# Optimization experiments

Measured on AMD Instinct MI355X. Metric: run time of the kernel, lower is better.

Reference implementation:

```python
import jax, jax.numpy as jnp
import numpy as np

N = 50000      # num_nodes
E = 800000     # num_edges (avg degree 16)
IN, HID, OUT = 128, 64, 64


def setup_inputs() -> dict:
    key = jax.random.key(0)
    ks = jax.random.split(key, 4)
    x = jax.random.normal(ks[0], (N, IN), dtype=jnp.float32)
    edge_index = jax.random.randint(ks[1], (2, E), 0, N, dtype=jnp.int32)
    # GCNConv params: weight [in, out] and bias [out] per layer
    W1 = jax.random.normal(ks[2], (IN, HID), dtype=jnp.float32) * 0.05
    b1 = jnp.zeros((HID,), dtype=jnp.float32)
    W2 = jax.random.normal(ks[3], (HID, OUT), dtype=jnp.float32) * 0.05
    b2 = jnp.zeros((OUT,), dtype=jnp.float32)
    return {"x": x, "edge_index": edge_index, "W1": W1, "b1": b1, "W2": W2, "b2": b2}


def _gcn_conv(x, W, b, src, dst, norm, n):
    # linear transform, then normalized gather->scatter-add aggregation
    h = x @ W                                    # [N, out]
    msg = h[src] * norm[:, None]                 # [E+N, out] gathered messages
    out = jax.ops.segment_sum(msg, dst, num_segments=n)
    return out + b


def reference(x, edge_index, W1, b1, W2, b2):
    n = x.shape[0]
    # add self-loops (PyG GCNConv default)
    loop = jnp.arange(n, dtype=edge_index.dtype)
    src = jnp.concatenate([edge_index[0], loop])
    dst = jnp.concatenate([edge_index[1], loop])
    # symmetric normalization D^-1/2 A D^-1/2 (degree over destination)
    deg = jax.ops.segment_sum(jnp.ones_like(dst, dtype=x.dtype), dst, num_segments=n)
    dinv = jnp.where(deg > 0, jax.lax.rsqrt(deg), jnp.zeros_like(deg))
    norm = dinv[src] * dinv[dst]                 # [E+N]
    h = _gcn_conv(x, W1, b1, src, dst, norm, n)
    h = jax.nn.leaky_relu(h, negative_slope=0.01)
    # dropout is identity in eval mode (training=False)
    return _gcn_conv(h, W2, b2, src, dst, norm, n)
```

## Files before the change

kernel.cpp:

```cpp
#include <hip/hip_runtime.h>
#include <hip/hip_fp16.h>
#include <type_traits>


#define NBC   128
#define BSH   7
#define NBMAX 512
#define CAP   8192

typedef __bf16 bf16x8 __attribute__((ext_vector_type(8)));
typedef float  f32x4  __attribute__((ext_vector_type(4)));

__device__ __forceinline__ unsigned short f2bf(float f) {
    unsigned u = __float_as_uint(f);
    unsigned r = u + 0x7fff + ((u >> 16) & 1);
    return (unsigned short)(r >> 16);
}
__device__ __forceinline__ float bf2f(unsigned short h) {
    return __uint_as_float(((unsigned)h) << 16);
}

__global__ __launch_bounds__(256) void k_hist1(const int* __restrict__ dst,
                                               int* __restrict__ T, int E, int nbuck) {
    __shared__ int hist[NBMAX];
    for (int i = threadIdx.x; i < nbuck; i += 256) hist[i] = 0;
    __syncthreads();
    const int per = (E + NBC - 1) / NBC;
    const int beg = blockIdx.x * per, end = min(beg + per, E);
    for (int i = beg + threadIdx.x; i < end; i += 256)
        atomicAdd(&hist[dst[i] >> BSH], 1);
    __syncthreads();
    for (int b = threadIdx.x; b < nbuck; b += 256)
        T[b * NBC + blockIdx.x] = hist[b];
}

__global__ __launch_bounds__(1024) void k_bsum(const int* __restrict__ in,
                                               int* __restrict__ bsum, int m) {
    __shared__ int red[16];
    const int t = threadIdx.x;
    const int i = blockIdx.x * 1024 + t;
    int v = (i < m) ? in[i] : 0;
#pragma unroll
    for (int o = 32; o; o >>= 1) v += __shfl_down(v, o);
    if ((t & 63) == 0) red[t >> 6] = v;
    __syncthreads();
    if (t == 0) {
        int s = 0;
#pragma unroll
        for (int w = 0; w < 16; ++w) s += red[w];
        bsum[blockIdx.x] = s;
    }
}

__global__ void k_sbsum(const int* __restrict__ bsum, int* __restrict__ boff, int nb) {
    if (threadIdx.x == 0 && blockIdx.x == 0) {
        int run = 0;
        for (int i = 0; i < nb; ++i) { boff[i] = run; run += bsum[i]; }
    }
}

__global__ __launch_bounds__(1024) void k_scanexc(
    const int* __restrict__ in, const int* __restrict__ boff,
    int* __restrict__ out, int m) {
    __shared__ int sh[1024];
    const int t = threadIdx.x;
    const int i = blockIdx.x * 1024 + t;
    const int v = (i < m) ? in[i] : 0;
    sh[t] = v;
    __syncthreads();
#pragma unroll
    for (int o = 1; o < 1024; o <<= 1) {
        int add = (t >= o) ? sh[t - o] : 0;
        __syncthreads();
        sh[t] += add;
        __syncthreads();
    }
    if (i < m) out[i] = boff[blockIdx.x] + sh[t] - v;
}

__global__ __launch_bounds__(256) void k_part1(
    const int* __restrict__ src, const int* __restrict__ dst,
    const int* __restrict__ Toff, unsigned* __restrict__ stage, int E, int nbuck) {
    __shared__ int base[NBMAX];
    __shared__ int cnt[NBMAX];
    for (int i = threadIdx.x; i < nbuck; i += 256) {
        base[i] = Toff[i * NBC + blockIdx.x];
        cnt[i] = 0;
    }
    __syncthreads();
    const int per = (E + NBC - 1) / NBC;
    const int beg = blockIdx.x * per, end = min(beg + per, E);
    for (int i = beg + threadIdx.x; i < end; i += 256) {
        int d = dst[i], s = src[i];
        int b = d >> BSH;
        int p = atomicAdd(&cnt[b], 1);
        stage[base[b] + p] = ((unsigned)(d & 127) << 17) | (unsigned)s;
    }
}

__global__ __launch_bounds__(256) void k_part2(
    const int* __restrict__ Toff, const unsigned* __restrict__ stage,
    int* __restrict__ csr, int* __restrict__ rowptr, float* __restrict__ dinv,
    int n, int E, int nbuck) {
    __shared__ unsigned buf[CAP];
    __shared__ unsigned srt[CAP];
    __shared__ int cnt[128], sc[128], curs[128];
    __shared__ int rbs, res;
    const int t = threadIdx.x;
    const int b = blockIdx.x;
    if (t < 128) cnt[t] = 0;
    if (t == 0) {
        rbs = Toff[b * NBC];
        res = (b == nbuck - 1) ? E : Toff[(b + 1) * NBC];
    }
    __syncthreads();
    const int rb = rbs, re = res, len = re - rb;
    if (len <= CAP) {
        for (int i = t; i < len; i += 256) {
            unsigned r = stage[rb + i];
            buf[i] = r;
            atomicAdd(&cnt[(r >> 17) & 127], 1);
        }
        __syncthreads();
        if (t < 128) sc[t] = cnt[t];
        __syncthreads();
#pragma unroll
        for (int o = 1; o < 128; o <<= 1) {
            int add = (t < 128 && t >= o) ? sc[t - o] : 0;
            __syncthreads();
            if (t < 128) sc[t] += add;
            __syncthreads();
        }
        if (t < 128) {
            curs[t] = sc[t] - cnt[t];
            const int gi = b * 128 + t;
            if (gi < n) {
                rowptr[gi] = rb + sc[t] - cnt[t];
                dinv[gi] = rsqrtf((float)cnt[t] + 1.f);
                if (gi == n - 1) rowptr[n] = rb + sc[t];
            }
        }
        __syncthreads();
        for (int i = t; i < len; i += 256) {
            unsigned r = buf[i];
            int p = atomicAdd(&curs[(r >> 17) & 127], 1);
            srt[p] = r & 0x1FFFF;
        }
        __syncthreads();
        for (int i = t; i < len; i += 256) csr[rb + i] = (int)srt[i];
    } else {
        for (int i = rb + t; i < re; i += 256)
            atomicAdd(&cnt[(stage[i] >> 17) & 127], 1);
        __syncthreads();
        if (t < 128) sc[t] = cnt[t];
        __syncthreads();
#pragma unroll
        for (int o = 1; o < 128; o <<= 1) {
            int add = (t < 128 && t >= o) ? sc[t - o] : 0;
            __syncthreads();
            if (t < 128) sc[t] += add;
            __syncthreads();
        }
        if (t < 128) {
            curs[t] = rb + sc[t] - cnt[t];
            const int gi = b * 128 + t;
            if (gi < n) {
                rowptr[gi] = rb + sc[t] - cnt[t];
                dinv[gi] = rsqrtf((float)cnt[t] + 1.f);
                if (gi == n - 1) rowptr[n] = rb + sc[t];
            }
        }
        __syncthreads();
        for (int i = rb + t; i < re; i += 256) {
            unsigned r = stage[i];
            int p = atomicAdd(&curs[(r >> 17) & 127], 1);
            csr[p] = (int)(r & 0x1FFFF);
        }
    }
}

__global__ void k_wsplit2(const float* __restrict__ W1, const float* __restrict__ W2,
                          unsigned short* __restrict__ W1s, unsigned short* __restrict__ W2s) {
    int i = blockIdx.x * blockDim.x + threadIdx.x;
    const float* W; unsigned short* out; int K, idx;
    if (i < 128 * 64)            { W = W1; out = W1s; K = 128; idx = i; }
    else if (i < 128 * 64 + 64 * 64) { W = W2; out = W2s; K = 64; idx = i - 128 * 64; }
    else return;
    int k = idx >> 6, c = idx & 63;
    float v = W[k * 64 + c];
    unsigned short hi = f2bf(v);
    unsigned short lo = f2bf(v - bf2f(hi));
    int T = K / 32;
    int t = k >> 5, kk = k & 31, g = kk >> 3, j = kk & 7;
    int ct = c >> 4, lane = g * 16 + (c & 15);
    out[(((size_t)(0 * T + t) * 4 + ct) * 64 + lane) * 8 + j] = hi;
    out[(((size_t)(1 * T + t) * 4 + ct) * 64 + lane) * 8 + j] = lo;
}

template<int K, bool LEAKY, typename AT>
__global__ __launch_bounds__(256) void k_gemm_mfma(
    const AT* __restrict__ A, const unsigned short* __restrict__ Ws,
    const float* __restrict__ dinv, __half* __restrict__ C, int n) {
    constexpr int T = K / 32;
    const int lane = threadIdx.x & 63;
    const int w = blockIdx.x * 4 + (threadIdx.x >> 6);
    const int r0 = w * 16;
    if (r0 >= n) return;
    const int g = lane >> 4, rA = lane & 15;

    bf16x8 ahi[T], alo[T];
    const AT* arow = A + (size_t)(r0 + rA) * K + g * 8;
#pragma unroll
    for (int t = 0; t < T; ++t) {
        float f[8];
        if constexpr (std::is_same<AT, float>::value) {
            float4 v0 = *(const float4*)(arow + t * 32);
            float4 v1 = *(const float4*)(arow + t * 32 + 4);
            f[0] = v0.x; f[1] = v0.y; f[2] = v0.z; f[3] = v0.w;
            f[4] = v1.x; f[5] = v1.y; f[6] = v1.z; f[7] = v1.w;
        } else {
            union { uint4 q; __half h[8]; } u;
            u.q = *(const uint4*)(arow + t * 32);
#pragma unroll
            for (int j = 0; j < 8; ++j) f[j] = __half2float(u.h[j]);
        }
        union { unsigned short u[8]; bf16x8 v; } H, L;
#pragma unroll
        for (int j = 0; j < 8; ++j) {
            float x = f[j];
            if (LEAKY) x = x > 0.f ? x : 0.01f * x;
            unsigned short h = f2bf(x);
            H.u[j] = h;
            L.u[j] = f2bf(x - bf2f(h));
        }
        ahi[t] = H.v; alo[t] = L.v;
    }

    f32x4 acc[4];
#pragma unroll
    for (int ct = 0; ct < 4; ++ct) acc[ct] = (f32x4){0.f, 0.f, 0.f, 0.f};

#pragma unroll
    for (int ct = 0; ct < 4; ++ct) {
#pragma unroll
        for (int t = 0; t < T; ++t) {
            union { uint4 q; bf16x8 v; } Bh, Bl;
            Bh.q = *(const uint4*)(Ws + (((size_t)(0 * T + t) * 4 + ct) * 64 + lane) * 8);
            Bl.q = *(const uint4*)(Ws + (((size_t)(1 * T + t) * 4 + ct) * 64 + lane) * 8);
            acc[ct] = __builtin_amdgcn_mfma_f32_16x16x32_bf16(ahi[t], Bh.v, acc[ct], 0, 0, 0);
            acc[ct] = __builtin_amdgcn_mfma_f32_16x16x32_bf16(ahi[t], Bl.v, acc[ct], 0, 0, 0);
            acc[ct] = __builtin_amdgcn_mfma_f32_16x16x32_bf16(alo[t], Bh.v, acc[ct], 0, 0, 0);
        }
    }

    float dv[4];
#pragma unroll
    for (int r = 0; r < 4; ++r) dv[r] = dinv[r0 + g * 4 + r];

    __half* crow = C + (size_t)(r0 + g * 4) * 64 + rA;
#pragma unroll
    for (int ct = 0; ct < 4; ++ct)
#pragma unroll
        for (int r = 0; r < 4; ++r)
            crow[(size_t)r * 64 + ct * 16] = __float2half_rn(acc[ct][r] * dv[r]);
}

template<typename OT>
__global__ __launch_bounds__(256) void k_aggcsr(
    const int* __restrict__ rowptr, const int* __restrict__ csr,
    const float* __restrict__ dinv, const __half* __restrict__ hs,
    const float* __restrict__ bias, OT* __restrict__ out, int n) {
    const int lane = threadIdx.x & 63;
    const int wid  = blockIdx.x * 4 + (threadIdx.x >> 6);
    const int nw   = gridDim.x * 4;
    const float bl = bias[lane];
    for (int dd = wid; dd < n; dd += nw) {
        const int d = __builtin_amdgcn_readfirstlane(dd);
        const int beg = rowptr[d], end = rowptr[d + 1];
        float a0 = 0.f, a1 = 0.f, a2 = 0.f, a3 = 0.f;
        float a4 = 0.f, a5 = 0.f, a6 = 0.f, a7 = 0.f;
        int j = beg;
        for (; j + 8 <= end; j += 8) {
            int s0 = csr[j + 0], s1 = csr[j + 1], s2 = csr[j + 2], s3 = csr[j + 3];
            int s4 = csr[j + 4], s5 = csr[j + 5], s6 = csr[j + 6], s7 = csr[j + 7];
            a0 += __half2float(hs[(size_t)s0 * 64 + lane]);
            a1 += __half2float(hs[(size_t)s1 * 64 + lane]);
            a2 += __half2float(hs[(size_t)s2 * 64 + lane]);
            a3 += __half2float(hs[(size_t)s3 * 64 + lane]);
            a4 += __half2float(hs[(size_t)s4 * 64 + lane]);
            a5 += __half2float(hs[(size_t)s5 * 64 + lane]);
            a6 += __half2float(hs[(size_t)s6 * 64 + lane]);
            a7 += __half2float(hs[(size_t)s7 * 64 + lane]);
        }
        for (; j < end; ++j)
            a0 += __half2float(hs[(size_t)csr[j] * 64 + lane]);
        const float di = dinv[d];
        const float acc = ((a0 + a1) + (a2 + a3)) + ((a4 + a5) + (a6 + a7));
        const float v = (acc + __half2float(hs[(size_t)d * 64 + lane])) * di + bl;
        if constexpr (std::is_same<OT, __half>::value)
            out[(size_t)d * 64 + lane] = __float2half_rn(v);
        else
            out[(size_t)d * 64 + lane] = v;
    }
}

extern "C" void kernel_launch(void* const* d_in, const int* in_sizes, int n_in,
                              void* d_out, int out_size, void* d_ws, size_t ws_size,
                              hipStream_t stream) {
    const float* x  = (const float*)d_in[0];
    const int*   ei = (const int*)d_in[1];
    const float* W1 = (const float*)d_in[2];
    const float* b1 = (const float*)d_in[3];
    const float* W2 = (const float*)d_in[4];
    const float* b2 = (const float*)d_in[5];
    float* out = (float*)d_out;

    const int n = in_sizes[0] / 128;
    const int E = in_sizes[1] / 2;
    const int* src = ei;
    const int* dst = ei + E;

    const int nbuck = (n + 127) >> BSH;
    const int m = nbuck * NBC;
    const int nb2 = (m + 1023) / 1024;

    char* ws = (char*)d_ws;
    size_t off = 0;
    auto alloc = [&](size_t bytes) { void* p = ws + off; off = (off + bytes + 255) & ~(size_t)255; return p; };
    int*      T      = (int*)alloc((size_t)m * 4);
    int*      Toff   = (int*)alloc((size_t)m * 4);
    int*      bsum   = (int*)alloc((size_t)nb2 * 4);
    int*      boff   = (int*)alloc((size_t)nb2 * 4);
    unsigned* stage  = (unsigned*)alloc((size_t)E * 4);
    int*      csr    = (int*)alloc((size_t)E * 4);
    int*      rowptr = (int*)alloc((size_t)(n + 1) * 4);
    float*    dinv   = (float*)alloc((size_t)n * 4);
    __half*   hs     = (__half*)alloc((size_t)n * 64 * 2);
    __half*   out1   = (__half*)alloc((size_t)n * 64 * 2);
    unsigned short* W1s = (unsigned short*)alloc((size_t)2 * 128 * 64 * 2);
    unsigned short* W2s = (unsigned short*)alloc((size_t)2 * 64 * 64 * 2);
    (void)ws_size; (void)n_in; (void)out_size;

    k_hist1  <<<NBC, 256, 0, stream>>>(dst, T, E, nbuck);
    k_bsum   <<<nb2, 1024, 0, stream>>>(T, bsum, m);
    k_sbsum  <<<1, 64, 0, stream>>>(bsum, boff, nb2);
    k_scanexc<<<nb2, 1024, 0, stream>>>(T, boff, Toff, m);
    k_part1  <<<NBC, 256, 0, stream>>>(src, dst, Toff, stage, E, nbuck);
    k_part2  <<<nbuck, 256, 0, stream>>>(Toff, stage, csr, rowptr, dinv, n, E, nbuck);

    k_wsplit2<<<(128 * 64 + 64 * 64 + 255) / 256, 256, 0, stream>>>(W1, W2, W1s, W2s);

    const int gemmBlocks = (n / 16 + 3) / 4;
    k_gemm_mfma<128, false, float><<<gemmBlocks, 256, 0, stream>>>(x, W1s, dinv, hs, n);
    k_aggcsr<__half><<<2048, 256, 0, stream>>>(rowptr, csr, dinv, hs, b1, out1, n);

    k_gemm_mfma<64, true, __half><<<gemmBlocks, 256, 0, stream>>>(out1, W2s, dinv, hs, n);
    k_aggcsr<float><<<2048, 256, 0, stream>>>(rowptr, csr, dinv, hs, b2, out, n);
}
```

Measured before the change: 111.3 us.

## Fuse weight split into histogram kernel, fold block-offset scan, vectorize partition loads

The weight hi/lo bf16 split now runs as extra blocks of the histogram kernel, and the serial block-sum scan kernel is folded into the exclusive-scan kernel, which recomputes its base from bsum in shared memory. Together these remove two kernel launches and the dependency gaps between them. The partition kernel now reads src and dst as int4 quads, with per-block chunks padded to a multiple of four. The aggregation loop gains a 4-wide remainder step, and the GEMM block count rounds up for n not divisible by 16.

```diff
diff --git a/kernel.cpp b/kernel.cpp
--- a/kernel.cpp
+++ b/kernel.cpp
@@ -20,12 +20,34 @@
     return __uint_as_float(((unsigned)h) << 16);
 }
 
-__global__ __launch_bounds__(256) void k_hist1(const int* __restrict__ dst,
-                                               int* __restrict__ T, int E, int nbuck) {
+__device__ __forceinline__ void wsplit_one(const float* __restrict__ W,
+                                           unsigned short* __restrict__ out,
+                                           int K, int idx) {
+    int k = idx >> 6, c = idx & 63;
+    float v = W[k * 64 + c];
+    unsigned short hi = f2bf(v);
+    unsigned short lo = f2bf(v - bf2f(hi));
+    int T = K / 32;
+    int t = k >> 5, kk = k & 31, g = kk >> 3, j = kk & 7;
+    int ct = c >> 4, lane = g * 16 + (c & 15);
+    out[(((size_t)(0 * T + t) * 4 + ct) * 64 + lane) * 8 + j] = hi;
+    out[(((size_t)(1 * T + t) * 4 + ct) * 64 + lane) * 8 + j] = lo;
+}
+
+__global__ __launch_bounds__(256) void k_hist_wsplit(
+    const int* __restrict__ dst, int* __restrict__ T, int E, int nbuck,
+    const float* __restrict__ W1, const float* __restrict__ W2,
+    unsigned short* __restrict__ W1s, unsigned short* __restrict__ W2s) {
     __shared__ int hist[NBMAX];
+    if (blockIdx.x >= NBC) {
+        int i = (blockIdx.x - NBC) * 256 + threadIdx.x;
+        if (i < 128 * 64) wsplit_one(W1, W1s, 128, i);
+        else if (i < 128 * 64 + 64 * 64) wsplit_one(W2, W2s, 64, i - 128 * 64);
+        return;
+    }
     for (int i = threadIdx.x; i < nbuck; i += 256) hist[i] = 0;
     __syncthreads();
-    const int per = (E + NBC - 1) / NBC;
+    const int per = (((E + NBC - 1) / NBC) + 3) & ~3;
     const int beg = blockIdx.x * per, end = min(beg + per, E);
     for (int i = beg + threadIdx.x; i < end; i += 256)
         atomicAdd(&hist[dst[i] >> BSH], 1);
@@ -52,22 +74,24 @@
     }
 }
 
-__global__ void k_sbsum(const int* __restrict__ bsum, int* __restrict__ boff, int nb) {
-    if (threadIdx.x == 0 && blockIdx.x == 0) {
-        int run = 0;
-        for (int i = 0; i < nb; ++i) { boff[i] = run; run += bsum[i]; }
-    }
-}
-
-__global__ __launch_bounds__(1024) void k_scanexc(
-    const int* __restrict__ in, const int* __restrict__ boff,
-    int* __restrict__ out, int m) {
+__global__ __launch_bounds__(1024) void k_scanexc2(
+    const int* __restrict__ in, const int* __restrict__ bsum,
+    int* __restrict__ out, int m, int nb) {
     __shared__ int sh[1024];
+    __shared__ int bb[64];
+    __shared__ int base;
     const int t = threadIdx.x;
     const int i = blockIdx.x * 1024 + t;
+    if (t < 64) bb[t] = (t < nb) ? bsum[t] : 0;
     const int v = (i < m) ? in[i] : 0;
     sh[t] = v;
     __syncthreads();
+    if (t == 0) {
+        int run = 0;
+        const int lim = blockIdx.x;
+        for (int k = 0; k < lim; ++k) run += bb[k];
+        base = run;
+    }
 #pragma unroll
     for (int o = 1; o < 1024; o <<= 1) {
         int add = (t >= o) ? sh[t - o] : 0;
@@ -75,7 +99,7 @@
         sh[t] += add;
         __syncthreads();
     }
-    if (i < m) out[i] = boff[blockIdx.x] + sh[t] - v;
+    if (i < m) out[i] = base + sh[t] - v;
 }
 
 __global__ __launch_bounds__(256) void k_part1(
@@ -88,9 +112,25 @@
         cnt[i] = 0;
     }
     __syncthreads();
-    const int per = (E + NBC - 1) / NBC;
+    const int per = (((E + NBC - 1) / NBC) + 3) & ~3;
     const int beg = blockIdx.x * per, end = min(beg + per, E);
-    for (int i = beg + threadIdx.x; i < end; i += 256) {
+    if (beg >= end) return;
+    const int nquad = (end - beg) >> 2;
+    for (int q = threadIdx.x; q < nquad; q += 256) {
+        const int i = beg + q * 4;
+        int4 s4 = *(const int4*)(src + i);
+        int4 d4 = *(const int4*)(dst + i);
+        int ss[4] = {s4.x, s4.y, s4.z, s4.w};
+        int dd[4] = {d4.x, d4.y, d4.z, d4.w};
+#pragma unroll
+        for (int k = 0; k < 4; ++k) {
+            int b = dd[k] >> BSH;
+            int p = atomicAdd(&cnt[b], 1);
+            stage[base[b] + p] = ((unsigned)(dd[k] & 127) << 17) | (unsigned)ss[k];
+        }
+    }
+    const int tb = beg + nquad * 4;
+    for (int i = tb + threadIdx.x; i < end; i += 256) {
         int d = dst[i], s = src[i];
         int b = d >> BSH;
         int p = atomicAdd(&cnt[b], 1);
@@ -179,24 +219,6 @@
     }
 }
 
-__global__ void k_wsplit2(const float* __restrict__ W1, const float* __restrict__ W2,
-                          unsigned short* __restrict__ W1s, unsigned short* __restrict__ W2s) {
-    int i = blockIdx.x * blockDim.x + threadIdx.x;
-    const float* W; unsigned short* out; int K, idx;
-    if (i < 128 * 64)            { W = W1; out = W1s; K = 128; idx = i; }
-    else if (i < 128 * 64 + 64 * 64) { W = W2; out = W2s; K = 64; idx = i - 128 * 64; }
-    else return;
-    int k = idx >> 6, c = idx & 63;
-    float v = W[k * 64 + c];
-    unsigned short hi = f2bf(v);
-    unsigned short lo = f2bf(v - bf2f(hi));
-    int T = K / 32;
-    int t = k >> 5, kk = k & 31, g = kk >> 3, j = kk & 7;
-    int ct = c >> 4, lane = g * 16 + (c & 15);
-    out[(((size_t)(0 * T + t) * 4 + ct) * 64 + lane) * 8 + j] = hi;
-    out[(((size_t)(1 * T + t) * 4 + ct) * 64 + lane) * 8 + j] = lo;
-}
-
 template<int K, bool LEAKY, typename AT>
 __global__ __launch_bounds__(256) void k_gemm_mfma(
     const AT* __restrict__ A, const unsigned short* __restrict__ Ws,
@@ -239,7 +261,6 @@
     f32x4 acc[4];
 #pragma unroll
     for (int ct = 0; ct < 4; ++ct) acc[ct] = (f32x4){0.f, 0.f, 0.f, 0.f};
-
 #pragma unroll
     for (int ct = 0; ct < 4; ++ct) {
 #pragma unroll
@@ -256,7 +277,6 @@
     float dv[4];
 #pragma unroll
     for (int r = 0; r < 4; ++r) dv[r] = dinv[r0 + g * 4 + r];
-
     __half* crow = C + (size_t)(r0 + g * 4) * 64 + rA;
 #pragma unroll
     for (int ct = 0; ct < 4; ++ct)
@@ -292,6 +312,13 @@
             a6 += __half2float(hs[(size_t)s6 * 64 + lane]);
             a7 += __half2float(hs[(size_t)s7 * 64 + lane]);
         }
+        for (; j + 4 <= end; j += 4) {
+            int s0 = csr[j + 0], s1 = csr[j + 1], s2 = csr[j + 2], s3 = csr[j + 3];
+            a0 += __half2float(hs[(size_t)s0 * 64 + lane]);
+            a1 += __half2float(hs[(size_t)s1 * 64 + lane]);
+            a2 += __half2float(hs[(size_t)s2 * 64 + lane]);
+            a3 += __half2float(hs[(size_t)s3 * 64 + lane]);
+        }
         for (; j < end; ++j)
             a0 += __half2float(hs[(size_t)csr[j] * 64 + lane]);
         const float di = dinv[d];
@@ -330,7 +357,6 @@
     int*      T      = (int*)alloc((size_t)m * 4);
     int*      Toff   = (int*)alloc((size_t)m * 4);
     int*      bsum   = (int*)alloc((size_t)nb2 * 4);
-    int*      boff   = (int*)alloc((size_t)nb2 * 4);
     unsigned* stage  = (unsigned*)alloc((size_t)E * 4);
     int*      csr    = (int*)alloc((size_t)E * 4);
     int*      rowptr = (int*)alloc((size_t)(n + 1) * 4);
@@ -341,16 +367,15 @@
     unsigned short* W2s = (unsigned short*)alloc((size_t)2 * 64 * 64 * 2);
     (void)ws_size; (void)n_in; (void)out_size;
 
-    k_hist1  <<<NBC, 256, 0, stream>>>(dst, T, E, nbuck);
-    k_bsum   <<<nb2, 1024, 0, stream>>>(T, bsum, m);
-    k_sbsum  <<<1, 64, 0, stream>>>(bsum, boff, nb2);
-    k_scanexc<<<nb2, 1024, 0, stream>>>(T, boff, Toff, m);
-    k_part1  <<<NBC, 256, 0, stream>>>(src, dst, Toff, stage, E, nbuck);
-    k_part2  <<<nbuck, 256, 0, stream>>>(Toff, stage, csr, rowptr, dinv, n, E, nbuck);
-
-    k_wsplit2<<<(128 * 64 + 64 * 64 + 255) / 256, 256, 0, stream>>>(W1, W2, W1s, W2s);
-
-    const int gemmBlocks = (n / 16 + 3) / 4;
+    const int wsplitBlocks = (128 * 64 + 64 * 64) / 256;
+
+    k_hist_wsplit<<<NBC + wsplitBlocks, 256, 0, stream>>>(dst, T, E, nbuck, W1, W2, W1s, W2s);
+    k_bsum    <<<nb2, 1024, 0, stream>>>(T, bsum, m);
+    k_scanexc2<<<nb2, 1024, 0, stream>>>(T, bsum, Toff, m, nb2);
+    k_part1   <<<NBC, 256, 0, stream>>>(src, dst, Toff, stage, E, nbuck);
+    k_part2   <<<nbuck, 256, 0, stream>>>(Toff, stage, csr, rowptr, dinv, n, E, nbuck);
+
+    const int gemmBlocks = ((n + 15) / 16 + 3) / 4;
     k_gemm_mfma<128, false, float><<<gemmBlocks, 256, 0, stream>>>(x, W1s, dinv, hs, n);
     k_aggcsr<__half><<<2048, 256, 0, stream>>>(rowptr, csr, dinv, hs, b1, out1, n);
 
```

After: 97.15 us, median of 2. -12.7%, faster.
